# Optimization experiments

Hardware: AMD Instinct MI355X
Metric: run time of the kernel (lower is better)

## Reference

```python
import jax, jax.numpy as jnp
import numpy as np

INNER_DIM = 64
HEAD_NUM = 8
D_MODEL = 512

def setup_inputs() -> dict:
    key = jax.random.key(0)
    k1, k2, k3 = jax.random.split(key, 3)
    x = jax.random.normal(k1, (4, 2048, D_MODEL), dtype=jnp.float32)
    # Keras 'uniform' initializer: U(-0.05, 0.05)
    kernel = jax.random.uniform(k2, (3 * HEAD_NUM, D_MODEL, INNER_DIM), dtype=jnp.float32, minval=-0.05, maxval=0.05)
    head_kernel = jax.random.uniform(k3, (INNER_DIM * HEAD_NUM, D_MODEL), dtype=jnp.float32, minval=-0.05, maxval=0.05)
    return {"x": x, "kernel": kernel, "head_kernel": head_kernel}

def reference(x, kernel, head_kernel):
    H, K = HEAD_NUM, INNER_DIM
    # kernel is interleaved per head: [Q0,K0,V0, Q1,K1,V1, ...]
    w = kernel.reshape(H, 3, kernel.shape[1], K)  # (H, 3, D, K)
    wq, wk, wv = w[:, 0], w[:, 1], w[:, 2]        # each (H, D, K)
    q = jnp.einsum('bsd,hdk->bhsk', x, wq)
    k = jnp.einsum('bsd,hdk->bhsk', x, wk)
    v = jnp.einsum('bsd,hdk->bhsk', x, wv)
    scores = jnp.einsum('bhsk,bhtk->bhst', q, k) / jnp.sqrt(jnp.asarray(K, x.dtype))
    probs = jax.nn.softmax(scores, axis=-1)
    o = jnp.einsum('bhst,bhtk->bhsk', probs, v)   # (B, H, S, K)
    B, _, S, _ = o.shape
    # concat over heads along last dim matches (B, S, H*K) with head-major order
    concated = jnp.transpose(o, (0, 2, 1, 3)).reshape(B, S, H * K)
    return jnp.einsum('bse,ed->bsd', concated, head_kernel)
```

## Files before the change

### kernel.cpp

```cpp
#include <hip/hip_runtime.h>
#include <math.h>

#define D_MODEL 512
#define INNER 64
#define HEADS 8
#define BATCH 4
#define SEQ 2048
#define BHN (BATCH*HEADS)
#define PER_MAT ((size_t)BHN*SEQ*INNER)

typedef __attribute__((ext_vector_type(8))) short short8;
typedef __attribute__((ext_vector_type(4))) float floatx4;

#if __has_builtin(__builtin_amdgcn_exp2f)
#define EXP2F(x) __builtin_amdgcn_exp2f(x)
#else
#define EXP2F(x) exp2f(x)
#endif

__device__ __forceinline__ void split_bf(float f, unsigned short& h, unsigned short& l) {
    unsigned int u = __float_as_uint(f);
    h = (unsigned short)(u >> 16);
    float hf = __uint_as_float(u & 0xffff0000u);
    l = (unsigned short)(__float_as_uint(f - hf) >> 16);
}

__device__ __forceinline__ void split4(const float* f, uint2& ph, uint2& pl) {
    unsigned int h[4], l[4];
#pragma unroll
    for (int j = 0; j < 4; ++j) {
        unsigned short hu, lu;
        split_bf(f[j], hu, lu);
        h[j] = hu; l[j] = lu;
    }
    ph.x = h[0] | (h[1] << 16); ph.y = h[2] | (h[3] << 16);
    pl.x = l[0] | (l[1] << 16); pl.y = l[2] | (l[3] << 16);
}

__global__ __launch_bounds__(256) void split_x(const float* __restrict__ X,
                                               unsigned short* __restrict__ Xh,
                                               unsigned short* __restrict__ Xl) {
    size_t base = ((size_t)blockIdx.x * 256 + threadIdx.x) * 8;
    float4 a = *(const float4*)&X[base];
    float4 b = *(const float4*)&X[base + 4];
    uint2 h0, l0, h1, l1;
    split4((const float*)&a, h0, l0);
    split4((const float*)&b, h1, l1);
    *(uint4*)&Xh[base] = make_uint4(h0.x, h0.y, h1.x, h1.y);
    *(uint4*)&Xl[base] = make_uint4(l0.x, l0.y, l1.x, l1.y);
}

__global__ __launch_bounds__(256) void split_w(const float* __restrict__ kern,
                                               unsigned short* __restrict__ Wth,
                                               unsigned short* __restrict__ Wtl) {
    __shared__ float tile[64 * 65];
    const int t = threadIdx.x;
    const int mat = blockIdx.x, k0 = blockIdx.y * 64;
#pragma unroll
    for (int c = 0; c < 4; ++c) {
        int idx = t + c * 256;
        int kl = idx >> 4, i4 = idx & 15;
        float4 v = *(const float4*)&kern[((size_t)mat * 512 + k0 + kl) * 64 + i4 * 4];
        tile[(i4 * 4 + 0) * 65 + kl] = v.x;
        tile[(i4 * 4 + 1) * 65 + kl] = v.y;
        tile[(i4 * 4 + 2) * 65 + kl] = v.z;
        tile[(i4 * 4 + 3) * 65 + kl] = v.w;
    }
    __syncthreads();
    {
        int i = t >> 2, kq = t & 3;
        uint2 h0, l0, h1, l1, h2, l2, h3, l3;
        float f[16];
#pragma unroll
        for (int jj = 0; jj < 16; ++jj) f[jj] = tile[i * 65 + kq * 16 + jj];
        split4(f, h0, l0); split4(f + 4, h1, l1);
        split4(f + 8, h2, l2); split4(f + 12, h3, l3);
        size_t off = ((size_t)mat * 64 + i) * 512 + k0 + kq * 16;
        *(uint4*)&Wth[off]     = make_uint4(h0.x, h0.y, h1.x, h1.y);
        *(uint4*)&Wth[off + 8] = make_uint4(h2.x, h2.y, h3.x, h3.y);
        *(uint4*)&Wtl[off]     = make_uint4(l0.x, l0.y, l1.x, l1.y);
        *(uint4*)&Wtl[off + 8] = make_uint4(l2.x, l2.y, l3.x, l3.y);
    }
}

__global__ __launch_bounds__(256) void split_hk(const float* __restrict__ HK,
                                                unsigned short* __restrict__ Hth,
                                                unsigned short* __restrict__ Htl) {
    __shared__ float tile[64 * 65];
    const int t = threadIdx.x;
    const int n0 = blockIdx.x * 64, k0 = blockIdx.y * 64;
#pragma unroll
    for (int c = 0; c < 4; ++c) {
        int idx = t + c * 256;
        int kl = idx >> 4, n4 = idx & 15;
        float4 v = *(const float4*)&HK[(size_t)(k0 + kl) * 512 + n0 + n4 * 4];
        tile[(n4 * 4 + 0) * 65 + kl] = v.x;
        tile[(n4 * 4 + 1) * 65 + kl] = v.y;
        tile[(n4 * 4 + 2) * 65 + kl] = v.z;
        tile[(n4 * 4 + 3) * 65 + kl] = v.w;
    }
    __syncthreads();
    {
        int i = t >> 2, kq = t & 3;
        uint2 h0, l0, h1, l1, h2, l2, h3, l3;
        float f[16];
#pragma unroll
        for (int jj = 0; jj < 16; ++jj) f[jj] = tile[i * 65 + kq * 16 + jj];
        split4(f, h0, l0); split4(f + 4, h1, l1);
        split4(f + 8, h2, l2); split4(f + 12, h3, l3);
        size_t off = (size_t)(n0 + i) * 512 + k0 + kq * 16;
        *(uint4*)&Hth[off]     = make_uint4(h0.x, h0.y, h1.x, h1.y);
        *(uint4*)&Hth[off + 8] = make_uint4(h2.x, h2.y, h3.x, h3.y);
        *(uint4*)&Htl[off]     = make_uint4(l0.x, l0.y, l1.x, l1.y);
        *(uint4*)&Htl[off + 8] = make_uint4(l2.x, l2.y, l3.x, l3.y);
    }
}

__global__ __launch_bounds__(256) __attribute__((amdgpu_waves_per_eu(3, 3)))
void qkv_mfma(const unsigned short* __restrict__ Xh,
              const unsigned short* __restrict__ Xl,
              const unsigned short* __restrict__ Wth,
              const unsigned short* __restrict__ Wtl,
              unsigned short* __restrict__ Qh,
              unsigned short* __restrict__ Ql,
              unsigned short* __restrict__ Kh,
              unsigned short* __restrict__ Kl,
              unsigned short* __restrict__ Vth,
              unsigned short* __restrict__ Vtl) {
    __shared__ __align__(16) unsigned short smem[16384];
    unsigned short* Ah = smem;
    unsigned short* Al = smem + 4096;
    unsigned short* Bh = smem + 8192;
    unsigned short* Bl = smem + 12288;

    const int t = threadIdx.x;
    const int w = t >> 6, lane = t & 63;
    const int quad = lane >> 4, l16 = lane & 15;
    const int wm = w & 1, wn = w >> 1;
    const int r0 = blockIdx.x * 128, n0 = blockIdx.y * 128;

    floatx4 acc[4][4];
#pragma unroll
    for (int mt = 0; mt < 4; ++mt)
#pragma unroll
        for (int nt = 0; nt < 4; ++nt) acc[mt][nt] = (floatx4)(0.f);

    for (int ko = 0; ko < 16; ++ko) {
        const int k0 = ko * 32;
        __syncthreads();
#pragma unroll
        for (int c = 0; c < 2; ++c) {
            int idx = t + c * 256;
            int row = idx >> 2, part = idx & 3;
            size_t src = (size_t)(r0 + row) * 512 + k0 + part * 8;
            *(uint4*)&Ah[row * 32 + part * 8] = *(const uint4*)&Xh[src];
            *(uint4*)&Al[row * 32 + part * 8] = *(const uint4*)&Xl[src];
        }
#pragma unroll
        for (int c = 0; c < 2; ++c) {
            int idx = t + c * 256;
            int n = idx >> 2, part = idx & 3;
            size_t src = (size_t)(n0 + n) * 512 + k0 + part * 8;
            *(uint4*)&Bh[n * 32 + part * 8] = *(const uint4*)&Wth[src];
            *(uint4*)&Bl[n * 32 + part * 8] = *(const uint4*)&Wtl[src];
        }
        __syncthreads();

        short8 af[4], alf[4], bf[4], blf[4];
#pragma unroll
        for (int mt = 0; mt < 4; ++mt) {
            af[mt]  = *(const short8*)&Ah[(wm * 64 + mt * 16 + l16) * 32 + quad * 8];
            alf[mt] = *(const short8*)&Al[(wm * 64 + mt * 16 + l16) * 32 + quad * 8];
        }
#pragma unroll
        for (int nt = 0; nt < 4; ++nt) {
            bf[nt]  = *(const short8*)&Bh[(wn * 64 + nt * 16 + l16) * 32 + quad * 8];
            blf[nt] = *(const short8*)&Bl[(wn * 64 + nt * 16 + l16) * 32 + quad * 8];
        }
#pragma unroll
        for (int mt = 0; mt < 4; ++mt)
#pragma unroll
            for (int nt = 0; nt < 4; ++nt) {
                acc[mt][nt] = __builtin_amdgcn_mfma_f32_16x16x32_bf16(af[mt], bf[nt], acc[mt][nt], 0, 0, 0);
                acc[mt][nt] = __builtin_amdgcn_mfma_f32_16x16x32_bf16(af[mt], blf[nt], acc[mt][nt], 0, 0, 0);
                acc[mt][nt] = __builtin_amdgcn_mfma_f32_16x16x32_bf16(alf[mt], bf[nt], acc[mt][nt], 0, 0, 0);
            }
    }

    __syncthreads();
    const int mat = (n0 + wn * 64) >> 6;
    const int h = mat / 3, j = mat - 3 * h;
    const size_t bh = (size_t)(r0 >> 11) * HEADS + h;
    float* pw = (float*)smem + w * 1088;
    const float scale = (j == 0) ? 0.18033688011112042f : 1.0f;

#pragma unroll
    for (int mt = 0; mt < 4; ++mt) {
        asm volatile("" ::: "memory");
#pragma unroll
        for (int nt = 0; nt < 4; ++nt)
#pragma unroll
            for (int r = 0; r < 4; ++r)
                pw[(quad * 4 + r) * 68 + nt * 16 + l16] = acc[mt][nt][r] * scale;
        asm volatile("s_waitcnt lgkmcnt(0)" ::: "memory");
        const int sbase = (r0 & 2047) + wm * 64 + mt * 16;
        if (j < 2) {
            unsigned short* dh = (j == 0) ? Qh : Kh;
            unsigned short* dl = (j == 0) ? Ql : Kl;
            float f[16];
            const float* pr = pw + l16 * 68 + quad * 16;
#pragma unroll
            for (int jj = 0; jj < 16; ++jj) f[jj] = pr[jj];
            uint2 h0, l0, h1, l1, h2, l2, h3, l3;
            split4(f, h0, l0); split4(f + 4, h1, l1);
            split4(f + 8, h2, l2); split4(f + 12, h3, l3);
            size_t off = (bh * SEQ + sbase + l16) * 64 + quad * 16;
            *(uint4*)&dh[off]     = make_uint4(h0.x, h0.y, h1.x, h1.y);
            *(uint4*)&dh[off + 8] = make_uint4(h2.x, h2.y, h3.x, h3.y);
            *(uint4*)&dl[off]     = make_uint4(l0.x, l0.y, l1.x, l1.y);
            *(uint4*)&dl[off + 8] = make_uint4(l2.x, l2.y, l3.x, l3.y);
        } else {
            float f[16];
#pragma unroll
            for (int ss = 0; ss < 16; ++ss) f[ss] = pw[ss * 68 + lane];
            uint2 h0, l0, h1, l1, h2, l2, h3, l3;
            split4(f, h0, l0); split4(f + 4, h1, l1);
            split4(f + 8, h2, l2); split4(f + 12, h3, l3);
            size_t bb = (bh * 64 + lane) * SEQ + (size_t)(sbase & ~31);
            const int a4 = (sbase & 16) ? 4 : 0;
            *(uint2*)&Vth[bb + a4]      = h0;
            *(uint2*)&Vth[bb + 8 + a4]  = h1;
            *(uint2*)&Vth[bb + 16 + a4] = h2;
            *(uint2*)&Vth[bb + 24 + a4] = h3;
            *(uint2*)&Vtl[bb + a4]      = l0;
            *(uint2*)&Vtl[bb + 8 + a4]  = l1;
            *(uint2*)&Vtl[bb + 16 + a4] = l2;
            *(uint2*)&Vtl[bb + 24 + a4] = l3;
        }
    }
}

__global__ __launch_bounds__(256) __attribute__((amdgpu_waves_per_eu(2, 2)))
void attn_mfma(
        const unsigned short* __restrict__ Qh_g, const unsigned short* __restrict__ Ql_g,
        const unsigned short* __restrict__ Kh_g, const unsigned short* __restrict__ Kl_g,
        const unsigned short* __restrict__ Vth_g, const unsigned short* __restrict__ Vtl_g,
        unsigned short* __restrict__ Oh_g, unsigned short* __restrict__ Ol_g) {
    __shared__ __align__(16) unsigned short smem[4 * 4608];
    unsigned short* Ksh = smem;
    unsigned short* Ksl = smem + 4608;
    unsigned short* Vsh = smem + 2 * 4608;
    unsigned short* Vsl = smem + 3 * 4608;

    const int t = threadIdx.x;
    const int w = t >> 6, lane = t & 63;
    const int quad = lane >> 4, l16 = lane & 15;
    const int bh = blockIdx.x;
    const int qbase = blockIdx.y * 128 + w * 32;

    short8 qhf[2][2], qlf[2][2];
#pragma unroll
    for (int qg = 0; qg < 2; ++qg) {
        const unsigned short* p = Qh_g + ((size_t)bh * SEQ + qbase + qg * 16 + l16) * INNER + quad * 8;
        qhf[qg][0] = *(const short8*)p;
        qhf[qg][1] = *(const short8*)(p + 32);
        const unsigned short* p2 = Ql_g + ((size_t)bh * SEQ + qbase + qg * 16 + l16) * INNER + quad * 8;
        qlf[qg][0] = *(const short8*)p2;
        qlf[qg][1] = *(const short8*)(p2 + 32);
    }

    floatx4 o[2][4];
#pragma unroll
    for (int qg = 0; qg < 2; ++qg)
#pragma unroll
        for (int nt = 0; nt < 4; ++nt) o[qg][nt] = (floatx4)(0.f);
    float mrun[2] = {-1e30f, -1e30f};
    float lrun[2] = {0.f, 0.f};

    const uint4* ksrc_h = (const uint4*)(Kh_g + (size_t)bh * SEQ * INNER);
    const uint4* ksrc_l = (const uint4*)(Kl_g + (size_t)bh * SEQ * INNER);
    const uint4* vsrc_h = (const uint4*)(Vth_g + (size_t)bh * INNER * SEQ);
    const uint4* vsrc_l = (const uint4*)(Vtl_g + (size_t)bh * INNER * SEQ);

    uint4 pkh[2], pkl[2], pvh[2], pvl[2];
#pragma unroll
    for (int ii = 0; ii < 2; ++ii) {
        int id = t + ii * 256, row = id >> 3, part = id & 7;
        pkh[ii] = ksrc_h[id];
        pkl[ii] = ksrc_l[id];
        pvh[ii] = vsrc_h[row * 256 + part];
        pvl[ii] = vsrc_l[row * 256 + part];
    }

    for (int kt = 0; kt < 32; ++kt) {
        __syncthreads();
#pragma unroll
        for (int ii = 0; ii < 2; ++ii) {
            int id = t + ii * 256, row = id >> 3, part = id & 7;
            int dst = row * 72 + part * 8;
            *(uint4*)&Ksh[dst] = pkh[ii];
            *(uint4*)&Ksl[dst] = pkl[ii];
            *(uint4*)&Vsh[dst] = pvh[ii];
            *(uint4*)&Vsl[dst] = pvl[ii];
        }
        __syncthreads();

        floatx4 s[2][4];
        __builtin_amdgcn_s_setprio(1);
#pragma unroll
        for (int st = 0; st < 4; ++st) {
            const unsigned short* ka = &Ksh[(st * 16 + l16) * 72 + quad * 8];
            const unsigned short* kb = &Ksl[(st * 16 + l16) * 72 + quad * 8];
            short8 kh0 = *(const short8*)ka;
            short8 kh1 = *(const short8*)(ka + 32);
            short8 kl0 = *(const short8*)kb;
            short8 kl1 = *(const short8*)(kb + 32);
#pragma unroll
            for (int qg = 0; qg < 2; ++qg) {
                floatx4 a = (floatx4)(0.f);
                a = __builtin_amdgcn_mfma_f32_16x16x32_bf16(kh0, qhf[qg][0], a, 0, 0, 0);
                a = __builtin_amdgcn_mfma_f32_16x16x32_bf16(kh1, qhf[qg][1], a, 0, 0, 0);
                a = __builtin_amdgcn_mfma_f32_16x16x32_bf16(kl0, qhf[qg][0], a, 0, 0, 0);
                a = __builtin_amdgcn_mfma_f32_16x16x32_bf16(kl1, qhf[qg][1], a, 0, 0, 0);
                a = __builtin_amdgcn_mfma_f32_16x16x32_bf16(kh0, qlf[qg][0], a, 0, 0, 0);
                a = __builtin_amdgcn_mfma_f32_16x16x32_bf16(kh1, qlf[qg][1], a, 0, 0, 0);
                s[qg][st] = a;
            }
        }
        __builtin_amdgcn_s_setprio(0);

        if (kt + 1 < 32) {
#pragma unroll
            for (int ii = 0; ii < 2; ++ii) {
                int id = t + ii * 256, row = id >> 3, part = id & 7;
                pkh[ii] = ksrc_h[(kt + 1) * 512 + id];
                pkl[ii] = ksrc_l[(kt + 1) * 512 + id];
                pvh[ii] = vsrc_h[row * 256 + (kt + 1) * 8 + part];
                pvl[ii] = vsrc_l[row * 256 + (kt + 1) * 8 + part];
            }
        }

#pragma unroll
        for (int qg = 0; qg < 2; ++qg) {
            float mloc = s[qg][0][0];
#pragma unroll
            for (int st = 0; st < 4; ++st)
#pragma unroll
                for (int r = 0; r < 4; ++r) mloc = fmaxf(mloc, s[qg][st][r]);
            mloc = fmaxf(mloc, __shfl_xor(mloc, 16));
            mloc = fmaxf(mloc, __shfl_xor(mloc, 32));
            if (!__all(mloc - mrun[qg] <= 8.f)) {
                float mn = fmaxf(mrun[qg], mloc);
                float alpha = EXP2F(mrun[qg] - mn);
                mrun[qg] = mn;
                lrun[qg] *= alpha;
#pragma unroll
                for (int nt = 0; nt < 4; ++nt) o[qg][nt] = o[qg][nt] * alpha;
            }
            float rs = 0.f;
#pragma unroll
            for (int st = 0; st < 4; ++st)
#pragma unroll
                for (int r = 0; r < 4; ++r) {
                    float p = EXP2F(s[qg][st][r] - mrun[qg]);
                    s[qg][st][r] = p;
                    rs += p;
                }
            rs += __shfl_xor(rs, 16);
            rs += __shfl_xor(rs, 32);
            lrun[qg] += rs;
        }

#pragma unroll
        for (int half = 0; half < 2; ++half) {
            short8 phf[2], plf[2];
#pragma unroll
            for (int qg = 0; qg < 2; ++qg)
#pragma unroll
                for (int j = 0; j < 8; ++j) {
                    unsigned short hu, lu;
                    split_bf(s[qg][2 * half + (j >> 2)][j & 3], hu, lu);
                    phf[qg][j] = (short)hu;
                    plf[qg][j] = (short)lu;
                }
            __builtin_amdgcn_s_setprio(1);
#pragma unroll
            for (int nt = 0; nt < 4; ++nt) {
                const unsigned short* va = &Vsh[(nt * 16 + l16) * 72 + half * 32 + quad * 8];
                const unsigned short* vb = &Vsl[(nt * 16 + l16) * 72 + half * 32 + quad * 8];
                short8 vh = *(const short8*)va;
                short8 vl = *(const short8*)vb;
#pragma unroll
                for (int qg = 0; qg < 2; ++qg) {
                    o[qg][nt] = __builtin_amdgcn_mfma_f32_16x16x32_bf16(vh, phf[qg], o[qg][nt], 0, 0, 0);
                    o[qg][nt] = __builtin_amdgcn_mfma_f32_16x16x32_bf16(vh, plf[qg], o[qg][nt], 0, 0, 0);
                    o[qg][nt] = __builtin_amdgcn_mfma_f32_16x16x32_bf16(vl, phf[qg], o[qg][nt], 0, 0, 0);
                }
            }
            __builtin_amdgcn_s_setprio(0);
        }
    }

    __syncthreads();
#pragma unroll
    for (int qg = 0; qg < 2; ++qg) {
        const float inv = 1.f / lrun[qg];
        float* pq = (float*)smem + (2 * w + qg) * 1088;
#pragma unroll
        for (int nt = 0; nt < 4; ++nt) {
            float4 v = make_float4(o[qg][nt][0] * inv, o[qg][nt][1] * inv,
                                   o[qg][nt][2] * inv, o[qg][nt][3] * inv);
            *(float4*)&pq[l16 * 68 + nt * 16 + quad * 4] = v;
        }
    }
    asm volatile("s_waitcnt lgkmcnt(0)" ::: "memory");
#pragma unroll
    for (int qg = 0; qg < 2; ++qg) {
        const float* pq = (const float*)smem + (2 * w + qg) * 1088 + l16 * 68 + quad * 16;
        float f[16];
#pragma unroll
        for (int jj = 0; jj < 16; ++jj) f[jj] = pq[jj];
        uint2 h0, l0, h1, l1, h2, l2, h3, l3;
        split4(f, h0, l0); split4(f + 4, h1, l1);
        split4(f + 8, h2, l2); split4(f + 12, h3, l3);
        size_t off = ((size_t)bh * SEQ + qbase + qg * 16 + l16) * 64 + quad * 16;
        *(uint4*)&Oh_g[off]     = make_uint4(h0.x, h0.y, h1.x, h1.y);
        *(uint4*)&Oh_g[off + 8] = make_uint4(h2.x, h2.y, h3.x, h3.y);
        *(uint4*)&Ol_g[off]     = make_uint4(l0.x, l0.y, l1.x, l1.y);
        *(uint4*)&Ol_g[off + 8] = make_uint4(l2.x, l2.y, l3.x, l3.y);
    }
}

__global__ __launch_bounds__(256) __attribute__((amdgpu_waves_per_eu(2, 2)))
void out_proj_mfma(const unsigned short* __restrict__ Oh,
                   const unsigned short* __restrict__ Ol,
                   const unsigned short* __restrict__ Hth,
                   const unsigned short* __restrict__ Htl,
                   float* __restrict__ Y) {
    __shared__ __align__(16) unsigned short smem[12288];
    unsigned short* Ah = smem;
    unsigned short* Al = smem + 2048;
    unsigned short* Bh = smem + 4096;
    unsigned short* Bl = smem + 8192;

    const int t = threadIdx.x;
    const int w = t >> 6, lane = t & 63;
    const int quad = lane >> 4, l16 = lane & 15;
    const int wm = w & 1, wn = w >> 1;
    const int r0 = blockIdx.x * 64, n0 = blockIdx.y * 128;
    const int b = r0 >> 11;

    floatx4 acc[2][4];
#pragma unroll
    for (int mt = 0; mt < 2; ++mt)
#pragma unroll
        for (int nt = 0; nt < 4; ++nt) acc[mt][nt] = (floatx4)(0.f);

    for (int ko = 0; ko < 16; ++ko) {
        const int h = ko >> 1, d0 = (ko & 1) * 32;
        const size_t bh = (size_t)b * HEADS + h;
        const int k0 = ko * 32;
        __syncthreads();
        {
            int row = t >> 2, part = t & 3;
            size_t src = (bh * SEQ + (r0 & 2047) + row) * 64 + d0 + part * 8;
            *(uint4*)&Ah[row * 32 + part * 8] = *(const uint4*)&Oh[src];
            *(uint4*)&Al[row * 32 + part * 8] = *(const uint4*)&Ol[src];
        }
#pragma unroll
        for (int c = 0; c < 2; ++c) {
            int idx = t + c * 256;
            int n = idx >> 2, part = idx & 3;
            size_t src = (size_t)(n0 + n) * 512 + k0 + part * 8;
            *(uint4*)&Bh[n * 32 + part * 8] = *(const uint4*)&Hth[src];
            *(uint4*)&Bl[n * 32 + part * 8] = *(const uint4*)&Htl[src];
        }
        __syncthreads();

        short8 af[2], alf[2], bf[4], blf[4];
#pragma unroll
        for (int mt = 0; mt < 2; ++mt) {
            af[mt]  = *(const short8*)&Ah[(wm * 32 + mt * 16 + l16) * 32 + quad * 8];
            alf[mt] = *(const short8*)&Al[(wm * 32 + mt * 16 + l16) * 32 + quad * 8];
        }
#pragma unroll
        for (int nt = 0; nt < 4; ++nt) {
            bf[nt]  = *(const short8*)&Bh[(wn * 64 + nt * 16 + l16) * 32 + quad * 8];
            blf[nt] = *(const short8*)&Bl[(wn * 64 + nt * 16 + l16) * 32 + quad * 8];
        }
#pragma unroll
        for (int mt = 0; mt < 2; ++mt)
#pragma unroll
            for (int nt = 0; nt < 4; ++nt) {
                acc[mt][nt] = __builtin_amdgcn_mfma_f32_16x16x32_bf16(af[mt], bf[nt], acc[mt][nt], 0, 0, 0);
                acc[mt][nt] = __builtin_amdgcn_mfma_f32_16x16x32_bf16(af[mt], blf[nt], acc[mt][nt], 0, 0, 0);
                acc[mt][nt] = __builtin_amdgcn_mfma_f32_16x16x32_bf16(alf[mt], bf[nt], acc[mt][nt], 0, 0, 0);
            }
    }

#pragma unroll
    for (int mt = 0; mt < 2; ++mt)
#pragma unroll
        for (int nt = 0; nt < 4; ++nt)
#pragma unroll
            for (int r = 0; r < 4; ++r)
                Y[(size_t)(r0 + wm * 32 + mt * 16 + quad * 4 + r) * 512 +
                  n0 + wn * 64 + nt * 16 + l16] = acc[mt][nt][r];
}

extern "C" void kernel_launch(void* const* d_in, const int* in_sizes, int n_in,
                              void* d_out, int out_size, void* d_ws, size_t ws_size,
                              hipStream_t stream) {
    const float* x    = (const float*)d_in[0];
    const float* kern = (const float*)d_in[1];
    const float* hk   = (const float*)d_in[2];
    float* y = (float*)d_out;

    unsigned short* Qh  = (unsigned short*)d_ws;
    unsigned short* Ql  = Qh + PER_MAT;
    unsigned short* Kh  = Qh + 2 * PER_MAT;
    unsigned short* Kl  = Qh + 3 * PER_MAT;
    unsigned short* Vth = Qh + 4 * PER_MAT;
    unsigned short* Vtl = Qh + 5 * PER_MAT;
    unsigned short* Oh  = Qh + 6 * PER_MAT;
    unsigned short* Ol  = Qh + 7 * PER_MAT;
    unsigned short* Xh  = Oh;
    unsigned short* Xl  = Ol;
    unsigned short* Wth = Qh + 8 * PER_MAT;
    unsigned short* Wtl = Wth + (size_t)1536 * 512;
    unsigned short* Hth = Wtl + (size_t)1536 * 512;
    unsigned short* Htl = Hth + (size_t)512 * 512;

    split_x<<<dim3(2048), 256, 0, stream>>>(x, Xh, Xl);
    split_w<<<dim3(24, 8), 256, 0, stream>>>(kern, Wth, Wtl);
    split_hk<<<dim3(8, 8), 256, 0, stream>>>(hk, Hth, Htl);
    qkv_mfma<<<dim3(64, 12), 256, 0, stream>>>(Xh, Xl, Wth, Wtl, Qh, Ql, Kh, Kl, Vth, Vtl);
    attn_mfma<<<dim3(32, 16), 256, 0, stream>>>(Qh, Ql, Kh, Kl, Vth, Vtl, Oh, Ol);
    out_proj_mfma<<<dim3(128, 4), 256, 0, stream>>>(Oh, Ol, Hth, Htl, y);
}
```

Before: 276.0 us.

## Stage two K/V tiles per barrier pair in attention kernel

The attention loop now loads two 64-key K/V tiles into registers at once, writes both into a doubled LDS buffer, and processes them between a single pair of barriers, halving the number of __syncthreads per pass. Prefetch of the next two tiles is issued after the first sub-tile's QK MFMAs. This doubles LDS use (about 73 KB) and the register prefetch buffers, which may lower occupancy under the fixed 2 waves-per-EU bound or cause spills.

```diff
diff --git a/kernel.cpp b/kernel.cpp
--- a/kernel.cpp
+++ b/kernel.cpp
@@ -246,11 +246,7 @@
         const unsigned short* __restrict__ Kh_g, const unsigned short* __restrict__ Kl_g,
         const unsigned short* __restrict__ Vth_g, const unsigned short* __restrict__ Vtl_g,
         unsigned short* __restrict__ Oh_g, unsigned short* __restrict__ Ol_g) {
-    __shared__ __align__(16) unsigned short smem[4 * 4608];
-    unsigned short* Ksh = smem;
-    unsigned short* Ksl = smem + 4608;
-    unsigned short* Vsh = smem + 2 * 4608;
-    unsigned short* Vsl = smem + 3 * 4608;
+    __shared__ __align__(16) unsigned short smem[8 * 4608];
 
     const int t = threadIdx.x;
     const int w = t >> 6, lane = t & 63;
@@ -282,124 +278,141 @@
     const uint4* vsrc_h = (const uint4*)(Vth_g + (size_t)bh * INNER * SEQ);
     const uint4* vsrc_l = (const uint4*)(Vtl_g + (size_t)bh * INNER * SEQ);
 
-    uint4 pkh[2], pkl[2], pvh[2], pvl[2];
-#pragma unroll
-    for (int ii = 0; ii < 2; ++ii) {
-        int id = t + ii * 256, row = id >> 3, part = id & 7;
-        pkh[ii] = ksrc_h[id];
-        pkl[ii] = ksrc_l[id];
-        pvh[ii] = vsrc_h[row * 256 + part];
-        pvl[ii] = vsrc_l[row * 256 + part];
-    }
-
-    for (int kt = 0; kt < 32; ++kt) {
+    uint4 pkh0[2], pkl0[2], pvh0[2], pvl0[2];
+    uint4 pkh1[2], pkl1[2], pvh1[2], pvl1[2];
+
+#define LOADSET(PH, PL, VH, VL, kt64) do {                                   \
+        _Pragma("unroll")                                                    \
+        for (int ii = 0; ii < 2; ++ii) {                                     \
+            int id = t + ii * 256, row = id >> 3, part = id & 7;             \
+            PH[ii] = ksrc_h[(kt64) * 512 + id];                              \
+            PL[ii] = ksrc_l[(kt64) * 512 + id];                              \
+            VH[ii] = vsrc_h[row * 256 + (kt64) * 8 + part];                  \
+            VL[ii] = vsrc_l[row * 256 + (kt64) * 8 + part];                  \
+        }                                                                    \
+    } while (0)
+
+#define WRITESET(PH, PL, VH, VL, base_) do {                                 \
+        _Pragma("unroll")                                                    \
+        for (int ii = 0; ii < 2; ++ii) {                                     \
+            int id = t + ii * 256, row = id >> 3, part = id & 7;             \
+            int dst = row * 72 + part * 8;                                   \
+            *(uint4*)&(base_)[dst]         = PH[ii];                         \
+            *(uint4*)&(base_)[dst + 4608]  = PL[ii];                         \
+            *(uint4*)&(base_)[dst + 9216]  = VH[ii];                         \
+            *(uint4*)&(base_)[dst + 13824] = VL[ii];                         \
+        }                                                                    \
+    } while (0)
+
+    LOADSET(pkh0, pkl0, pvh0, pvl0, 0);
+    LOADSET(pkh1, pkl1, pvh1, pvl1, 1);
+
+    for (int ht = 0; ht < 16; ++ht) {
         __syncthreads();
-#pragma unroll
-        for (int ii = 0; ii < 2; ++ii) {
-            int id = t + ii * 256, row = id >> 3, part = id & 7;
-            int dst = row * 72 + part * 8;
-            *(uint4*)&Ksh[dst] = pkh[ii];
-            *(uint4*)&Ksl[dst] = pkl[ii];
-            *(uint4*)&Vsh[dst] = pvh[ii];
-            *(uint4*)&Vsl[dst] = pvl[ii];
-        }
+        WRITESET(pkh0, pkl0, pvh0, pvl0, smem);
+        WRITESET(pkh1, pkl1, pvh1, pvl1, smem + 18432);
         __syncthreads();
 
-        floatx4 s[2][4];
-        __builtin_amdgcn_s_setprio(1);
-#pragma unroll
-        for (int st = 0; st < 4; ++st) {
-            const unsigned short* ka = &Ksh[(st * 16 + l16) * 72 + quad * 8];
-            const unsigned short* kb = &Ksl[(st * 16 + l16) * 72 + quad * 8];
-            short8 kh0 = *(const short8*)ka;
-            short8 kh1 = *(const short8*)(ka + 32);
-            short8 kl0 = *(const short8*)kb;
-            short8 kl1 = *(const short8*)(kb + 32);
-#pragma unroll
-            for (int qg = 0; qg < 2; ++qg) {
-                floatx4 a = (floatx4)(0.f);
-                a = __builtin_amdgcn_mfma_f32_16x16x32_bf16(kh0, qhf[qg][0], a, 0, 0, 0);
-                a = __builtin_amdgcn_mfma_f32_16x16x32_bf16(kh1, qhf[qg][1], a, 0, 0, 0);
-                a = __builtin_amdgcn_mfma_f32_16x16x32_bf16(kl0, qhf[qg][0], a, 0, 0, 0);
-                a = __builtin_amdgcn_mfma_f32_16x16x32_bf16(kl1, qhf[qg][1], a, 0, 0, 0);
-                a = __builtin_amdgcn_mfma_f32_16x16x32_bf16(kh0, qlf[qg][0], a, 0, 0, 0);
-                a = __builtin_amdgcn_mfma_f32_16x16x32_bf16(kh1, qlf[qg][1], a, 0, 0, 0);
-                s[qg][st] = a;
-            }
-        }
-        __builtin_amdgcn_s_setprio(0);
-
-        if (kt + 1 < 32) {
-#pragma unroll
-            for (int ii = 0; ii < 2; ++ii) {
-                int id = t + ii * 256, row = id >> 3, part = id & 7;
-                pkh[ii] = ksrc_h[(kt + 1) * 512 + id];
-                pkl[ii] = ksrc_l[(kt + 1) * 512 + id];
-                pvh[ii] = vsrc_h[row * 256 + (kt + 1) * 8 + part];
-                pvl[ii] = vsrc_l[row * 256 + (kt + 1) * 8 + part];
-            }
-        }
-
-#pragma unroll
-        for (int qg = 0; qg < 2; ++qg) {
-            float mloc = s[qg][0][0];
-#pragma unroll
-            for (int st = 0; st < 4; ++st)
-#pragma unroll
-                for (int r = 0; r < 4; ++r) mloc = fmaxf(mloc, s[qg][st][r]);
-            mloc = fmaxf(mloc, __shfl_xor(mloc, 16));
-            mloc = fmaxf(mloc, __shfl_xor(mloc, 32));
-            if (!__all(mloc - mrun[qg] <= 8.f)) {
-                float mn = fmaxf(mrun[qg], mloc);
-                float alpha = EXP2F(mrun[qg] - mn);
-                mrun[qg] = mn;
-                lrun[qg] *= alpha;
-#pragma unroll
-                for (int nt = 0; nt < 4; ++nt) o[qg][nt] = o[qg][nt] * alpha;
-            }
-            float rs = 0.f;
-#pragma unroll
-            for (int st = 0; st < 4; ++st)
-#pragma unroll
-                for (int r = 0; r < 4; ++r) {
-                    float p = EXP2F(s[qg][st][r] - mrun[qg]);
-                    s[qg][st][r] = p;
-                    rs += p;
-                }
-            rs += __shfl_xor(rs, 16);
-            rs += __shfl_xor(rs, 32);
-            lrun[qg] += rs;
-        }
-
-#pragma unroll
-        for (int half = 0; half < 2; ++half) {
-            short8 phf[2], plf[2];
-#pragma unroll
-            for (int qg = 0; qg < 2; ++qg)
-#pragma unroll
-                for (int j = 0; j < 8; ++j) {
-                    unsigned short hu, lu;
-                    split_bf(s[qg][2 * half + (j >> 2)][j & 3], hu, lu);
-                    phf[qg][j] = (short)hu;
-                    plf[qg][j] = (short)lu;
-                }
+#pragma unroll
+        for (int sub = 0; sub < 2; ++sub) {
+            const unsigned short* Ksh = smem + sub * 18432;
+            const unsigned short* Ksl = Ksh + 4608;
+            const unsigned short* Vsh = Ksh + 9216;
+            const unsigned short* Vsl = Ksh + 13824;
+
+            floatx4 s[2][4];
             __builtin_amdgcn_s_setprio(1);
 #pragma unroll
-            for (int nt = 0; nt < 4; ++nt) {
-                const unsigned short* va = &Vsh[(nt * 16 + l16) * 72 + half * 32 + quad * 8];
-                const unsigned short* vb = &Vsl[(nt * 16 + l16) * 72 + half * 32 + quad * 8];
-                short8 vh = *(const short8*)va;
-                short8 vl = *(const short8*)vb;
+            for (int st = 0; st < 4; ++st) {
+                const unsigned short* ka = &Ksh[(st * 16 + l16) * 72 + quad * 8];
+                const unsigned short* kb = &Ksl[(st * 16 + l16) * 72 + quad * 8];
+                short8 kh0 = *(const short8*)ka;
+                short8 kh1 = *(const short8*)(ka + 32);
+                short8 kl0 = *(const short8*)kb;
+                short8 kl1 = *(const short8*)(kb + 32);
 #pragma unroll
                 for (int qg = 0; qg < 2; ++qg) {
-                    o[qg][nt] = __builtin_amdgcn_mfma_f32_16x16x32_bf16(vh, phf[qg], o[qg][nt], 0, 0, 0);
-                    o[qg][nt] = __builtin_amdgcn_mfma_f32_16x16x32_bf16(vh, plf[qg], o[qg][nt], 0, 0, 0);
-                    o[qg][nt] = __builtin_amdgcn_mfma_f32_16x16x32_bf16(vl, phf[qg], o[qg][nt], 0, 0, 0);
+                    floatx4 a = (floatx4)(0.f);
+                    a = __builtin_amdgcn_mfma_f32_16x16x32_bf16(kh0, qhf[qg][0], a, 0, 0, 0);
+                    a = __builtin_amdgcn_mfma_f32_16x16x32_bf16(kh1, qhf[qg][1], a, 0, 0, 0);
+                    a = __builtin_amdgcn_mfma_f32_16x16x32_bf16(kl0, qhf[qg][0], a, 0, 0, 0);
+                    a = __builtin_amdgcn_mfma_f32_16x16x32_bf16(kl1, qhf[qg][1], a, 0, 0, 0);
+                    a = __builtin_amdgcn_mfma_f32_16x16x32_bf16(kh0, qlf[qg][0], a, 0, 0, 0);
+                    a = __builtin_amdgcn_mfma_f32_16x16x32_bf16(kh1, qlf[qg][1], a, 0, 0, 0);
+                    s[qg][st] = a;
                 }
             }
             __builtin_amdgcn_s_setprio(0);
-        }
-    }
+
+            if (sub == 0 && ht + 1 < 16) {
+                LOADSET(pkh0, pkl0, pvh0, pvl0, 2 * ht + 2);
+                LOADSET(pkh1, pkl1, pvh1, pvl1, 2 * ht + 3);
+            }
+
+#pragma unroll
+            for (int qg = 0; qg < 2; ++qg) {
+                float mloc = s[qg][0][0];
+#pragma unroll
+                for (int st = 0; st < 4; ++st)
+#pragma unroll
+                    for (int r = 0; r < 4; ++r) mloc = fmaxf(mloc, s[qg][st][r]);
+                mloc = fmaxf(mloc, __shfl_xor(mloc, 16));
+                mloc = fmaxf(mloc, __shfl_xor(mloc, 32));
+                if (!__all(mloc - mrun[qg] <= 8.f)) {
+                    float mn = fmaxf(mrun[qg], mloc);
+                    float alpha = EXP2F(mrun[qg] - mn);
+                    mrun[qg] = mn;
+                    lrun[qg] *= alpha;
+#pragma unroll
+                    for (int nt = 0; nt < 4; ++nt) o[qg][nt] = o[qg][nt] * alpha;
+                }
+                float rs = 0.f;
+#pragma unroll
+                for (int st = 0; st < 4; ++st)
+#pragma unroll
+                    for (int r = 0; r < 4; ++r) {
+                        float p = EXP2F(s[qg][st][r] - mrun[qg]);
+                        s[qg][st][r] = p;
+                        rs += p;
+                    }
+                rs += __shfl_xor(rs, 16);
+                rs += __shfl_xor(rs, 32);
+                lrun[qg] += rs;
+            }
+
+#pragma unroll
+            for (int half = 0; half < 2; ++half) {
+                short8 phf[2], plf[2];
+#pragma unroll
+                for (int qg = 0; qg < 2; ++qg)
+#pragma unroll
+                    for (int j = 0; j < 8; ++j) {
+                        unsigned short hu, lu;
+                        split_bf(s[qg][2 * half + (j >> 2)][j & 3], hu, lu);
+                        phf[qg][j] = (short)hu;
+                        plf[qg][j] = (short)lu;
+                    }
+                __builtin_amdgcn_s_setprio(1);
+#pragma unroll
+                for (int nt = 0; nt < 4; ++nt) {
+                    const unsigned short* va = &Vsh[(nt * 16 + l16) * 72 + half * 32 + quad * 8];
+                    const unsigned short* vb = &Vsl[(nt * 16 + l16) * 72 + half * 32 + quad * 8];
+                    short8 vh = *(const short8*)va;
+                    short8 vl = *(const short8*)vb;
+#pragma unroll
+                    for (int qg = 0; qg < 2; ++qg) {
+                        o[qg][nt] = __builtin_amdgcn_mfma_f32_16x16x32_bf16(vh, phf[qg], o[qg][nt], 0, 0, 0);
+                        o[qg][nt] = __builtin_amdgcn_mfma_f32_16x16x32_bf16(vh, plf[qg], o[qg][nt], 0, 0, 0);
+                        o[qg][nt] = __builtin_amdgcn_mfma_f32_16x16x32_bf16(vl, phf[qg], o[qg][nt], 0, 0, 0);
+                    }
+                }
+                __builtin_amdgcn_s_setprio(0);
+            }
+        }
+    }
+
+#undef LOADSET
+#undef WRITESET
 
     __syncthreads();
 #pragma unroll
```

Result: slower. 343.5 us (+24.5%).
